# Performance work log

Hardware: AMD Instinct MI355X
Metric: run time of the kernel (lower is better)

## Reference

```python
import jax, jax.numpy as jnp
import numpy as np

D_MODEL = 512
N_HEAD = 8


def setup_inputs() -> dict:
    key = jax.random.key(0)
    ks = jax.random.split(key, 9)
    s = 1.0 / np.sqrt(D_MODEL)
    inp = {
        "x": jax.random.normal(ks[0], (2, 4096, D_MODEL), dtype=jnp.float32),
        "wq": jax.random.uniform(ks[1], (D_MODEL, D_MODEL), jnp.float32, -s, s),
        "bq": jax.random.uniform(ks[2], (D_MODEL,), jnp.float32, -s, s),
        "wk": jax.random.uniform(ks[3], (D_MODEL, D_MODEL), jnp.float32, -s, s),
        "bk": jax.random.uniform(ks[4], (D_MODEL,), jnp.float32, -s, s),
        "wv": jax.random.uniform(ks[5], (D_MODEL, D_MODEL), jnp.float32, -s, s),
        "bv": jax.random.uniform(ks[6], (D_MODEL,), jnp.float32, -s, s),
        "wo": jax.random.uniform(ks[7], (D_MODEL, D_MODEL), jnp.float32, -s, s),
        "bo": jax.random.uniform(ks[8], (D_MODEL,), jnp.float32, -s, s),
    }
    return inp


def reference(x, wq, bq, wk, bk, wv, bv, wo, bo):
    B, S, D = x.shape
    H = N_HEAD
    Dh = D // H

    def split_heads(t):  # [B,S,D] -> [B,H,S,Dh]
        return t.reshape(B, S, H, Dh).transpose(0, 2, 1, 3)

    q = split_heads(x @ wq.T + bq)
    k = split_heads(x @ wk.T + bk)
    v = split_heads(x @ wv.T + bv)

    # explicit (unfused) attention, matching the torch module
    score = jnp.einsum("bhsd,bhtd->bhst", q, k) / jnp.sqrt(jnp.float32(Dh))
    attn = jax.nn.softmax(score, axis=-1)
    out = jnp.einsum("bhst,bhtd->bhsd", attn, v)  # [B,H,S,Dh]

    out = out.transpose(0, 2, 1, 3).reshape(B, S, D)
    return out @ wo.T + bo
```

## Files before the change

### kernel.cpp

```cpp
#include <hip/hip_runtime.h>
#include <math.h>

#define S_LEN 4096
#define DMODEL 512
#define NHEAD 8
#define E_ELEMS ((size_t)8192 * 512)
#define QSCALE 0.18033688f

typedef __attribute__((ext_vector_type(8))) short bf16x8;
typedef __attribute__((ext_vector_type(4))) float f32x4;
typedef __attribute__((ext_vector_type(16))) float f32x16;
typedef unsigned short u16;
typedef unsigned int u32;

__device__ __forceinline__ u16 f2bf(float f) {
    u32 u = __float_as_uint(f);
    u += 0x7FFFu + ((u >> 16) & 1u);
    return (u16)(u >> 16);
}
__device__ __forceinline__ float bf2f(u16 h) {
    return __uint_as_float((u32)h << 16);
}

#define MFMA16(a, b, c) __builtin_amdgcn_mfma_f32_16x16x32_bf16((a), (b), (c), 0, 0, 0)
#define MFMA32(a, b, c) __builtin_amdgcn_mfma_f32_32x32x16_bf16((a), (b), (c), 0, 0, 0)

__global__ __launch_bounds__(256) void cvt_x(const float* __restrict__ in,
                                             u16* __restrict__ out, int n4) {
    const int i = blockIdx.x * 256 + threadIdx.x;
    if (i >= n4) return;
    const float4 v = ((const float4*)in)[i];
    uint2 hp;
    hp.x = (u32)f2bf(v.x) | ((u32)f2bf(v.y) << 16);
    hp.y = (u32)f2bf(v.z) | ((u32)f2bf(v.w) << 16);
    ((uint2*)out)[i] = hp;
}

__global__ __launch_bounds__(256) void cvt_w(
    const float* __restrict__ wq, const float* __restrict__ wk,
    const float* __restrict__ wv, const float* __restrict__ wo,
    u16* __restrict__ oq, u16* __restrict__ ok,
    u16* __restrict__ ov, u16* __restrict__ oo) {
    const int i = blockIdx.x * 256 + threadIdx.x;
    {
        const float4 v = ((const float4*)wq)[i];
        uint2 hp;
        hp.x = (u32)f2bf(v.x * QSCALE) | ((u32)f2bf(v.y * QSCALE) << 16);
        hp.y = (u32)f2bf(v.z * QSCALE) | ((u32)f2bf(v.w * QSCALE) << 16);
        ((uint2*)oq)[i] = hp;
    }
    {
        const float4 v = ((const float4*)wk)[i];
        uint2 hp;
        hp.x = (u32)f2bf(v.x) | ((u32)f2bf(v.y) << 16);
        hp.y = (u32)f2bf(v.z) | ((u32)f2bf(v.w) << 16);
        ((uint2*)ok)[i] = hp;
    }
    {
        const float4 v = ((const float4*)wv)[i];
        uint2 hp;
        hp.x = (u32)f2bf(v.x) | ((u32)f2bf(v.y) << 16);
        hp.y = (u32)f2bf(v.z) | ((u32)f2bf(v.w) << 16);
        ((uint2*)ov)[i] = hp;
    }
    {
        const float4 v = ((const float4*)wo)[i];
        uint2 hp;
        hp.x = (u32)f2bf(v.x) | ((u32)f2bf(v.y) << 16);
        hp.y = (u32)f2bf(v.z) | ((u32)f2bf(v.w) << 16);
        ((uint2*)oo)[i] = hp;
    }
}

template<int MODE>
__global__ __launch_bounds__(256) void proj2_kernel(
    const u16* __restrict__ Abf,
    const u16* __restrict__ W0, const float* __restrict__ Bi0,
    const u16* __restrict__ W1, const float* __restrict__ Bi1,
    u16* __restrict__ Qo, u16* __restrict__ Ko, float* __restrict__ Out)
{
    __shared__ __align__(16) u16 sm[16384];
    u16* As = sm;
    u16* Bs = sm + 8192;

    const int tid = threadIdx.x;
    const int w = tid >> 6, l = tid & 63, g = (l >> 4), c = l & 15;
    const int wr = w >> 1, wc = w & 1;
    const int bm = blockIdx.x * 128;
    const int n0 = blockIdx.y * 128;
    const int z = (MODE == 0) ? blockIdx.z : 0;
    const u16* W   = z ? W1 : W0;
    const float* Bi = z ? Bi1 : Bi0;
    const float bsc = (MODE == 0 && z == 0) ? QSCALE : 1.0f;

    const int sr = l >> 3;
    const int slot = l & 7;

    f32x4 acc[4][4];
    #pragma unroll
    for (int i = 0; i < 4; ++i)
        #pragma unroll
        for (int j = 0; j < 4; ++j) acc[i][j] = (f32x4){0.f, 0.f, 0.f, 0.f};

    #pragma unroll 1
    for (int kt = 0; kt < 8; ++kt) {
        const int k0 = kt * 64;
        __syncthreads();
        #pragma unroll
        for (int i = 0; i < 4; ++i) {
            const int row = i * 32 + w * 8 + sr;
            const int scol = (slot ^ (row & 7)) * 8;
            __builtin_amdgcn_global_load_lds(
                Abf + (size_t)(bm + row) * DMODEL + k0 + scol,
                As + (i * 32 + w * 8) * 64, 16, 0, 0);
            __builtin_amdgcn_global_load_lds(
                W + (size_t)(n0 + row) * DMODEL + k0 + scol,
                Bs + (i * 32 + w * 8) * 64, 16, 0, 0);
        }
        __syncthreads();

        #pragma unroll
        for (int kc = 0; kc < 2; ++kc) {
            bf16x8 a[4], b[4];
            #pragma unroll
            for (int mf = 0; mf < 4; ++mf) {
                const int ra = wr * 64 + mf * 16 + c;
                a[mf] = *(const bf16x8*)(As + ra * 64 + (((kc * 4 + g) ^ (ra & 7)) * 8));
            }
            #pragma unroll
            for (int nf = 0; nf < 4; ++nf) {
                const int rb = wc * 64 + nf * 16 + c;
                b[nf] = *(const bf16x8*)(Bs + rb * 64 + (((kc * 4 + g) ^ (rb & 7)) * 8));
            }
            #pragma unroll
            for (int mf = 0; mf < 4; ++mf)
                #pragma unroll
                for (int nf = 0; nf < 4; ++nf)
                    acc[mf][nf] = MFMA16(a[mf], b[nf], acc[mf][nf]);
        }
    }

    #pragma unroll
    for (int mf = 0; mf < 4; ++mf)
        #pragma unroll
        for (int nf = 0; nf < 4; ++nf) {
            const int n = n0 + wc * 64 + nf * 16 + c;
            const float bias = Bi[n] * bsc;
            #pragma unroll
            for (int r = 0; r < 4; ++r) {
                const int m = bm + wr * 64 + mf * 16 + 4 * g + r;
                const float v = acc[mf][nf][r] + bias;
                if (MODE == 1) {
                    Out[(size_t)m * DMODEL + n] = v;
                } else {
                    const int b = m >> 12, s = m & (S_LEN - 1);
                    const int hh = n >> 6, dd = n & 63;
                    const size_t o = ((size_t)((b * NHEAD + hh) * S_LEN + s)) * 64 + dd;
                    if (z == 0) Qo[o] = f2bf(v);
                    else        Ko[o] = f2bf(v);
                }
            }
        }
}

__global__ __launch_bounds__(256) void proj_v_kernel(
    const u16* __restrict__ Abf, const u16* __restrict__ Wv,
    const float* __restrict__ Bv, u16* __restrict__ Vt)
{
    __shared__ __align__(16) u16 sm[18432];
    u16* Ah = sm;
    u16* Bh = sm + 9216;

    const int tid = threadIdx.x;
    const int w = tid >> 6, lane = tid & 63, g = lane >> 4, c = lane & 15;
    const int bm = blockIdx.x * 128;
    const int n0 = blockIdx.y * 64;

    f32x4 acc[2][4];
    #pragma unroll
    for (int a = 0; a < 2; ++a)
        #pragma unroll
        for (int b = 0; b < 4; ++b) acc[a][b] = (f32x4){0.f, 0.f, 0.f, 0.f};

    #pragma unroll 1
    for (int kt = 0; kt < 8; ++kt) {
        const int k0 = kt * 64;
        __syncthreads();
        #pragma unroll
        for (int i = 0; i < 4; ++i) {
            const int slot = i * 256 + tid;
            const int r = slot >> 3, c8 = slot & 7;
            *(uint4*)(Ah + r * 72 + c8 * 8) =
                *(const uint4*)(Abf + (size_t)(bm + r) * DMODEL + k0 + c8 * 8);
        }
        #pragma unroll
        for (int i = 0; i < 2; ++i) {
            const int slot = i * 256 + tid;
            const int r = slot >> 3, c8 = slot & 7;
            *(uint4*)(Bh + r * 72 + c8 * 8) =
                *(const uint4*)(Wv + (size_t)(n0 + r) * DMODEL + k0 + c8 * 8);
        }
        __syncthreads();

        #pragma unroll
        for (int kc = 0; kc < 2; ++kc) {
            bf16x8 a[2], b[4];
            #pragma unroll
            for (int mf = 0; mf < 2; ++mf)
                a[mf] = *(const bf16x8*)(Ah + (w * 32 + mf * 16 + c) * 72 + kc * 32 + g * 8);
            #pragma unroll
            for (int nf = 0; nf < 4; ++nf)
                b[nf] = *(const bf16x8*)(Bh + (nf * 16 + c) * 72 + kc * 32 + g * 8);
            #pragma unroll
            for (int mf = 0; mf < 2; ++mf)
                #pragma unroll
                for (int nf = 0; nf < 4; ++nf)
                    acc[mf][nf] = MFMA16(a[mf], b[nf], acc[mf][nf]);
        }
    }

    __syncthreads();
    float* scr = (float*)sm;
    #pragma unroll
    for (int mf = 0; mf < 2; ++mf)
        #pragma unroll
        for (int nf = 0; nf < 4; ++nf) {
            const float bias = Bv[n0 + nf * 16 + c];
            #pragma unroll
            for (int r = 0; r < 4; ++r)
                scr[(w * 32 + mf * 16 + 4 * g + r) * 72 + nf * 16 + c] =
                    acc[mf][nf][r] + bias;
        }
    __syncthreads();
    const int d = tid & 63, sb = tid >> 6;
    const int b = bm >> 12, h = n0 >> 6;
    const size_t obase =
        ((size_t)((b * NHEAD + h) * 64 + d)) * S_LEN + (bm & (S_LEN - 1)) + sb * 32;
    u16 th[32];
    #pragma unroll
    for (int j = 0; j < 32; ++j)
        th[j] = f2bf(scr[(sb * 32 + j) * 72 + d]);
    #pragma unroll
    for (int q = 0; q < 4; ++q)
        *(uint4*)(Vt + obase + q * 8) = *(const uint4*)&th[q * 8];
}

__global__ __launch_bounds__(256, 2) void attn_kernel(
    const u16* __restrict__ Qb, const u16* __restrict__ Kb,
    const u16* __restrict__ Vt, u16* __restrict__ OpB, float* __restrict__ Lp)
{
    __shared__ __align__(16) u16 sm[16384];

    const int tid = threadIdx.x;
    const int w = tid >> 6, l = tid & 63;
    const int r0 = l & 31, hi = l >> 5;

    const int f = blockIdx.x;
    const int wg = (f & 7) * 128 + (f >> 3);
    const int bh = wg >> 6, kvq = (wg >> 4) & 3, qb = wg & 15;
    const int b = bh >> 3, h = bh & 7;

    const size_t hoff = (size_t)bh * S_LEN * 64;
    const int qw = qb * 256 + w * 64;
    const int kv0 = kvq * 1024;

    bf16x8 qf[2][4];
    #pragma unroll
    for (int qfi = 0; qfi < 2; ++qfi)
        #pragma unroll
        for (int kc = 0; kc < 4; ++kc)
            qf[qfi][kc] = *(const bf16x8*)(Qb + hoff +
                (size_t)(qw + qfi * 32 + r0) * 64 + kc * 16 + hi * 8);

    const int rbase = r0 * 64;
    int soff[4];
    #pragma unroll
    for (int j = 0; j < 4; ++j) soff[j] = ((2 * j + hi) ^ (r0 & 7)) * 8;

    const int srow0 = w * 16 + (l >> 3);
    const int slot  = l & 7;
    const int srow1 = srow0 + 8;
    const u16* srcK0 = Kb + hoff + (size_t)(kv0 + srow0) * 64 + ((slot ^ (srow0 & 7)) * 8);
    const u16* srcK1 = Kb + hoff + (size_t)(kv0 + srow1) * 64 + ((slot ^ (srow1 & 7)) * 8);
    const u16* srcV0 = Vt + ((size_t)bh * 64 + srow0) * S_LEN + kv0 + ((slot ^ (srow0 & 7)) * 8);
    const u16* srcV1 = Vt + ((size_t)bh * 64 + srow1) * S_LEN + kv0 + ((slot ^ (srow1 & 7)) * 8);

#define STAGE(bufb, t) do {                                                        \
        u16* kb_ = sm + (bufb) * 8192 + w * 1024;                                  \
        u16* vb_ = kb_ + 4096;                                                     \
        __builtin_amdgcn_global_load_lds(srcK0 + (size_t)(t) * 4096, kb_,       16, 0, 0); \
        __builtin_amdgcn_global_load_lds(srcK1 + (size_t)(t) * 4096, kb_ + 512, 16, 0, 0); \
        __builtin_amdgcn_global_load_lds(srcV0 + (size_t)(t) * 64,   vb_,       16, 0, 0); \
        __builtin_amdgcn_global_load_lds(srcV1 + (size_t)(t) * 64,   vb_ + 512, 16, 0, 0); \
    } while (0)

#define ZERO16 {0.f,0.f,0.f,0.f,0.f,0.f,0.f,0.f,0.f,0.f,0.f,0.f,0.f,0.f,0.f,0.f}
    f32x16 o00 = ZERO16, o01 = ZERO16, o10 = ZERO16, o11 = ZERO16;
    f32x16 laccA = ZERO16, laccB = ZERO16;

    STAGE(0, 0);
    __syncthreads();
    int buf = 0;

    #pragma unroll 1
    for (int t = 0; t < 16; ++t) {
        if (t + 1 < 16) STAGE(buf ^ 1, t + 1);

        const u16* Kb_s = sm + buf * 8192;
        const u16* Vb_s = Kb_s + 4096;

        bf16x8 pa0[4], pa1[4];
        #pragma unroll
        for (int kvf = 0; kvf < 2; ++kvf) {
            f32x16 sA = ZERO16, sB = ZERO16;
            __builtin_amdgcn_s_setprio(1);
            #pragma unroll
            for (int kc = 0; kc < 4; ++kc) {
                const bf16x8 k = *(const bf16x8*)(Kb_s + kvf * 2048 + rbase + soff[kc]);
                sA = MFMA32(k, qf[0][kc], sA);
                sB = MFMA32(k, qf[1][kc], sB);
            }
            __builtin_amdgcn_s_setprio(0);
            #pragma unroll
            for (int r = 0; r < 16; ++r) {
                sA[r] = __builtin_amdgcn_exp2f(sA[r]);
                sB[r] = __builtin_amdgcn_exp2f(sB[r]);
            }
            laccA += sA;
            laccB += sB;
            #pragma unroll
            for (int hf = 0; hf < 2; ++hf) {
                const int rb = hf * 8;
                u32 x0, y0, x1, y1;
                asm("v_cvt_pk_bf16_f32 %0, %1, %2" : "=v"(x0) : "v"(sA[rb+0]), "v"(sA[rb+1]));
                asm("v_cvt_pk_bf16_f32 %0, %1, %2" : "=v"(y0) : "v"(sA[rb+4]), "v"(sA[rb+5]));
                asm("v_cvt_pk_bf16_f32 %0, %1, %2" : "=v"(x1) : "v"(sA[rb+2]), "v"(sA[rb+3]));
                asm("v_cvt_pk_bf16_f32 %0, %1, %2" : "=v"(y1) : "v"(sA[rb+6]), "v"(sA[rb+7]));
                asm volatile("v_permlane32_swap_b32 %0, %1" : "+v"(x0), "+v"(y0));
                asm volatile("v_permlane32_swap_b32 %0, %1" : "+v"(x1), "+v"(y1));
                union { u32 u[4]; bf16x8 v; } PA;
                PA.u[0] = x0; PA.u[1] = x1; PA.u[2] = y0; PA.u[3] = y1;
                pa0[kvf * 2 + hf] = PA.v;
                asm("v_cvt_pk_bf16_f32 %0, %1, %2" : "=v"(x0) : "v"(sB[rb+0]), "v"(sB[rb+1]));
                asm("v_cvt_pk_bf16_f32 %0, %1, %2" : "=v"(y0) : "v"(sB[rb+4]), "v"(sB[rb+5]));
                asm("v_cvt_pk_bf16_f32 %0, %1, %2" : "=v"(x1) : "v"(sB[rb+2]), "v"(sB[rb+3]));
                asm("v_cvt_pk_bf16_f32 %0, %1, %2" : "=v"(y1) : "v"(sB[rb+6]), "v"(sB[rb+7]));
                asm volatile("v_permlane32_swap_b32 %0, %1" : "+v"(x0), "+v"(y0));
                asm volatile("v_permlane32_swap_b32 %0, %1" : "+v"(x1), "+v"(y1));
                union { u32 u[4]; bf16x8 v; } PB;
                PB.u[0] = x0; PB.u[1] = x1; PB.u[2] = y0; PB.u[3] = y1;
                pa1[kvf * 2 + hf] = PB.v;
            }
        }

        __builtin_amdgcn_s_setprio(1);
        #pragma unroll
        for (int kvc = 0; kvc < 4; ++kvc) {
            const bf16x8 v0 = *(const bf16x8*)(Vb_s + rbase + soff[kvc]);
            const bf16x8 v1 = *(const bf16x8*)(Vb_s + 2048 + rbase + soff[kvc]);
            o00 = MFMA32(pa0[kvc], v0, o00);
            o01 = MFMA32(pa0[kvc], v1, o01);
            o10 = MFMA32(pa1[kvc], v0, o10);
            o11 = MFMA32(pa1[kvc], v1, o11);
        }
        __builtin_amdgcn_s_setprio(0);

        __syncthreads();
        buf ^= 1;
    }
#undef STAGE

    float l0 = 0.f, l1 = 0.f;
    #pragma unroll
    for (int r = 0; r < 16; ++r) { l0 += laccA[r]; l1 += laccB[r]; }
    l0 += __shfl_xor(l0, 32);
    l1 += __shfl_xor(l1, 32);
    if (hi == 0) {
        Lp[((size_t)kvq * 16 + bh) * S_LEN + qw + r0]      = l0;
        Lp[((size_t)kvq * 16 + bh) * S_LEN + qw + 32 + r0] = l1;
    }

    u16* Ob = OpB + (size_t)kvq * E_ELEMS + (size_t)b * S_LEN * DMODEL;
    #pragma unroll
    for (int qfi = 0; qfi < 2; ++qfi)
        #pragma unroll
        for (int df = 0; df < 2; ++df) {
            #pragma unroll
            for (int r = 0; r < 16; ++r) {
                const float ov = qfi ? (df ? o11[r] : o10[r]) : (df ? o01[r] : o00[r]);
                const int q = qfi * 32 + (r & 3) + 8 * (r >> 2) + 4 * hi;
                Ob[(size_t)(qw + q) * DMODEL + h * 64 + df * 32 + r0] = f2bf(ov);
            }
        }
}

__global__ __launch_bounds__(256) void combine_kernel(
    const u16* __restrict__ Op, const float* __restrict__ Lp,
    u16* __restrict__ A)
{
    const int i = blockIdx.x * 256 + threadIdx.x;
    const int m = i >> 6;
    const int col = (i & 63) * 8;
    const int b = m >> 12, s = m & (S_LEN - 1), h = col >> 6;
    const int bh = b * 8 + h;

    float lt = 0.f;
    #pragma unroll
    for (int kq = 0; kq < 4; ++kq)
        lt += Lp[((size_t)kq * 16 + bh) * S_LEN + s];
    const float inv = 1.0f / lt;

    float acc[8] = {};
    #pragma unroll
    for (int kq = 0; kq < 4; ++kq) {
        const uint4 v = *(const uint4*)(Op + (size_t)kq * E_ELEMS + (size_t)m * DMODEL + col);
        const u16* p = (const u16*)&v;
        #pragma unroll
        for (int j = 0; j < 8; ++j) acc[j] += bf2f(p[j]);
    }
    u16 r[8];
    #pragma unroll
    for (int j = 0; j < 8; ++j) r[j] = f2bf(acc[j] * inv);
    *(uint4*)(A + (size_t)m * DMODEL + col) = *(const uint4*)r;
}

extern "C" void kernel_launch(void* const* d_in, const int* in_sizes, int n_in,
                              void* d_out, int out_size, void* d_ws, size_t ws_size,
                              hipStream_t stream)
{
    const float* x  = (const float*)d_in[0];
    const float* wq = (const float*)d_in[1];
    const float* bq = (const float*)d_in[2];
    const float* wk = (const float*)d_in[3];
    const float* bk = (const float*)d_in[4];
    const float* wv = (const float*)d_in[5];
    const float* bv = (const float*)d_in[6];
    const float* wo = (const float*)d_in[7];
    const float* bo = (const float*)d_in[8];

    u16* ws = (u16*)d_ws;
    const size_t E = E_ELEMS;
    u16* xbf  = ws;
    u16* Qbf  = ws + E;
    u16* Kbf  = ws + 2 * E;
    u16* Vtbf = ws + 3 * E;
    u16* wqbf = ws + 4 * E;
    u16* wkbf = wqbf + DMODEL * DMODEL;
    u16* wvbf = wkbf + DMODEL * DMODEL;
    u16* wobf = wvbf + DMODEL * DMODEL;
    u16* OpB  = wobf + DMODEL * DMODEL;
    float* Lp = (float*)(OpB + 4 * E);

    cvt_x<<<dim3(4096), 256, 0, stream>>>(x, xbf, (int)(E / 4));
    cvt_w<<<dim3(256), 256, 0, stream>>>(wq, wk, wv, wo, wqbf, wkbf, wvbf, wobf);

    proj2_kernel<0><<<dim3(64, 4, 2), 256, 0, stream>>>(
        xbf, wqbf, bq, wkbf, bk, Qbf, Kbf, nullptr);

    proj_v_kernel<<<dim3(64, 8), 256, 0, stream>>>(xbf, wvbf, bv, Vtbf);

    attn_kernel<<<dim3(1024), 256, 0, stream>>>(Qbf, Kbf, Vtbf, OpB, Lp);

    combine_kernel<<<dim3(2048), 256, 0, stream>>>(OpB, Lp, xbf);

    proj2_kernel<1><<<dim3(64, 4), 256, 0, stream>>>(
        xbf, wobf, bo, nullptr, nullptr, nullptr, nullptr, (float*)d_out);
}
```

Baseline: 139.4 us.

## Merge conversion kernels, fold V projection into QK GEMM, interleave PV MFMAs

```diff
diff --git a/kernel.cpp b/kernel.cpp
--- a/kernel.cpp
+++ b/kernel.cpp
@@ -25,50 +25,51 @@
 #define MFMA16(a, b, c) __builtin_amdgcn_mfma_f32_16x16x32_bf16((a), (b), (c), 0, 0, 0)
 #define MFMA32(a, b, c) __builtin_amdgcn_mfma_f32_32x32x16_bf16((a), (b), (c), 0, 0, 0)
 
-__global__ __launch_bounds__(256) void cvt_x(const float* __restrict__ in,
-                                             u16* __restrict__ out, int n4) {
-    const int i = blockIdx.x * 256 + threadIdx.x;
-    if (i >= n4) return;
-    const float4 v = ((const float4*)in)[i];
-    uint2 hp;
-    hp.x = (u32)f2bf(v.x) | ((u32)f2bf(v.y) << 16);
-    hp.y = (u32)f2bf(v.z) | ((u32)f2bf(v.w) << 16);
-    ((uint2*)out)[i] = hp;
-}
-
-__global__ __launch_bounds__(256) void cvt_w(
+__global__ __launch_bounds__(256) void cvt_all(
+    const float* __restrict__ x,
     const float* __restrict__ wq, const float* __restrict__ wk,
     const float* __restrict__ wv, const float* __restrict__ wo,
-    u16* __restrict__ oq, u16* __restrict__ ok,
-    u16* __restrict__ ov, u16* __restrict__ oo) {
-    const int i = blockIdx.x * 256 + threadIdx.x;
-    {
-        const float4 v = ((const float4*)wq)[i];
-        uint2 hp;
-        hp.x = (u32)f2bf(v.x * QSCALE) | ((u32)f2bf(v.y * QSCALE) << 16);
-        hp.y = (u32)f2bf(v.z * QSCALE) | ((u32)f2bf(v.w * QSCALE) << 16);
-        ((uint2*)oq)[i] = hp;
-    }
-    {
-        const float4 v = ((const float4*)wk)[i];
+    u16* __restrict__ xbf, u16* __restrict__ oq, u16* __restrict__ ok,
+    u16* __restrict__ ov, u16* __restrict__ oo)
+{
+    const int bid = blockIdx.x;
+    if (bid < 4096) {
+        const int i = bid * 256 + threadIdx.x;
+        const float4 v = ((const float4*)x)[i];
         uint2 hp;
         hp.x = (u32)f2bf(v.x) | ((u32)f2bf(v.y) << 16);
         hp.y = (u32)f2bf(v.z) | ((u32)f2bf(v.w) << 16);
-        ((uint2*)ok)[i] = hp;
-    }
-    {
-        const float4 v = ((const float4*)wv)[i];
-        uint2 hp;
-        hp.x = (u32)f2bf(v.x) | ((u32)f2bf(v.y) << 16);
-        hp.y = (u32)f2bf(v.z) | ((u32)f2bf(v.w) << 16);
-        ((uint2*)ov)[i] = hp;
-    }
-    {
-        const float4 v = ((const float4*)wo)[i];
-        uint2 hp;
-        hp.x = (u32)f2bf(v.x) | ((u32)f2bf(v.y) << 16);
-        hp.y = (u32)f2bf(v.z) | ((u32)f2bf(v.w) << 16);
-        ((uint2*)oo)[i] = hp;
+        ((uint2*)xbf)[i] = hp;
+    } else {
+        const int i = (bid - 4096) * 256 + threadIdx.x;
+        {
+            const float4 v = ((const float4*)wq)[i];
+            uint2 hp;
+            hp.x = (u32)f2bf(v.x * QSCALE) | ((u32)f2bf(v.y * QSCALE) << 16);
+            hp.y = (u32)f2bf(v.z * QSCALE) | ((u32)f2bf(v.w * QSCALE) << 16);
+            ((uint2*)oq)[i] = hp;
+        }
+        {
+            const float4 v = ((const float4*)wk)[i];
+            uint2 hp;
+            hp.x = (u32)f2bf(v.x) | ((u32)f2bf(v.y) << 16);
+            hp.y = (u32)f2bf(v.z) | ((u32)f2bf(v.w) << 16);
+            ((uint2*)ok)[i] = hp;
+        }
+        {
+            const float4 v = ((const float4*)wv)[i];
+            uint2 hp;
+            hp.x = (u32)f2bf(v.x) | ((u32)f2bf(v.y) << 16);
+            hp.y = (u32)f2bf(v.z) | ((u32)f2bf(v.w) << 16);
+            ((uint2*)ov)[i] = hp;
+        }
+        {
+            const float4 v = ((const float4*)wo)[i];
+            uint2 hp;
+            hp.x = (u32)f2bf(v.x) | ((u32)f2bf(v.y) << 16);
+            hp.y = (u32)f2bf(v.z) | ((u32)f2bf(v.w) << 16);
+            ((uint2*)oo)[i] = hp;
+        }
     }
 }
 
@@ -77,9 +78,11 @@
     const u16* __restrict__ Abf,
     const u16* __restrict__ W0, const float* __restrict__ Bi0,
     const u16* __restrict__ W1, const float* __restrict__ Bi1,
-    u16* __restrict__ Qo, u16* __restrict__ Ko, float* __restrict__ Out)
+    const u16* __restrict__ W2, const float* __restrict__ Bi2,
+    u16* __restrict__ Qo, u16* __restrict__ Ko, u16* __restrict__ Vt,
+    float* __restrict__ Out)
 {
-    __shared__ __align__(16) u16 sm[16384];
+    __shared__ __align__(16) u16 sm[18432];
     u16* As = sm;
     u16* Bs = sm + 8192;
 
@@ -89,8 +92,8 @@
     const int bm = blockIdx.x * 128;
     const int n0 = blockIdx.y * 128;
     const int z = (MODE == 0) ? blockIdx.z : 0;
-    const u16* W   = z ? W1 : W0;
-    const float* Bi = z ? Bi1 : Bi0;
+    const u16* W   = (z == 0) ? W0 : (z == 1) ? W1 : W2;
+    const float* Bi = (z == 0) ? Bi0 : (z == 1) ? Bi1 : Bi2;
     const float bsc = (MODE == 0 && z == 0) ? QSCALE : 1.0f;
 
     const int sr = l >> 3;
@@ -138,6 +141,41 @@
                 for (int nf = 0; nf < 4; ++nf)
                     acc[mf][nf] = MFMA16(a[mf], b[nf], acc[mf][nf]);
         }
+    }
+
+    if (MODE == 0 && z == 2) {
+        __syncthreads();
+        float* scr = (float*)sm;
+        const int d = tid & 63, sb = tid >> 6;
+        const int b = bm >> 12;
+        #pragma unroll
+        for (int pass = 0; pass < 2; ++pass) {
+            if (wc == pass) {
+                #pragma unroll
+                for (int mf = 0; mf < 4; ++mf)
+                    #pragma unroll
+                    for (int nf = 0; nf < 4; ++nf) {
+                        const float bias = Bi[n0 + pass * 64 + nf * 16 + c];
+                        #pragma unroll
+                        for (int r = 0; r < 4; ++r)
+                            scr[(wr * 64 + mf * 16 + 4 * g + r) * 72 + nf * 16 + c] =
+                                acc[mf][nf][r] + bias;
+                    }
+            }
+            __syncthreads();
+            const int hh = (n0 >> 6) + pass;
+            const size_t obase =
+                ((size_t)((b * NHEAD + hh) * 64 + d)) * S_LEN + (bm & (S_LEN - 1)) + sb * 32;
+            u16 th[32];
+            #pragma unroll
+            for (int j = 0; j < 32; ++j)
+                th[j] = f2bf(scr[(sb * 32 + j) * 72 + d]);
+            #pragma unroll
+            for (int q4 = 0; q4 < 4; ++q4)
+                *(uint4*)(Vt + obase + q4 * 8) = *(const uint4*)&th[q4 * 8];
+            __syncthreads();
+        }
+        return;
     }
 
     #pragma unroll
@@ -163,88 +201,6 @@
         }
 }
 
-__global__ __launch_bounds__(256) void proj_v_kernel(
-    const u16* __restrict__ Abf, const u16* __restrict__ Wv,
-    const float* __restrict__ Bv, u16* __restrict__ Vt)
-{
-    __shared__ __align__(16) u16 sm[18432];
-    u16* Ah = sm;
-    u16* Bh = sm + 9216;
-
-    const int tid = threadIdx.x;
-    const int w = tid >> 6, lane = tid & 63, g = lane >> 4, c = lane & 15;
-    const int bm = blockIdx.x * 128;
-    const int n0 = blockIdx.y * 64;
-
-    f32x4 acc[2][4];
-    #pragma unroll
-    for (int a = 0; a < 2; ++a)
-        #pragma unroll
-        for (int b = 0; b < 4; ++b) acc[a][b] = (f32x4){0.f, 0.f, 0.f, 0.f};
-
-    #pragma unroll 1
-    for (int kt = 0; kt < 8; ++kt) {
-        const int k0 = kt * 64;
-        __syncthreads();
-        #pragma unroll
-        for (int i = 0; i < 4; ++i) {
-            const int slot = i * 256 + tid;
-            const int r = slot >> 3, c8 = slot & 7;
-            *(uint4*)(Ah + r * 72 + c8 * 8) =
-                *(const uint4*)(Abf + (size_t)(bm + r) * DMODEL + k0 + c8 * 8);
-        }
-        #pragma unroll
-        for (int i = 0; i < 2; ++i) {
-            const int slot = i * 256 + tid;
-            const int r = slot >> 3, c8 = slot & 7;
-            *(uint4*)(Bh + r * 72 + c8 * 8) =
-                *(const uint4*)(Wv + (size_t)(n0 + r) * DMODEL + k0 + c8 * 8);
-        }
-        __syncthreads();
-
-        #pragma unroll
-        for (int kc = 0; kc < 2; ++kc) {
-            bf16x8 a[2], b[4];
-            #pragma unroll
-            for (int mf = 0; mf < 2; ++mf)
-                a[mf] = *(const bf16x8*)(Ah + (w * 32 + mf * 16 + c) * 72 + kc * 32 + g * 8);
-            #pragma unroll
-            for (int nf = 0; nf < 4; ++nf)
-                b[nf] = *(const bf16x8*)(Bh + (nf * 16 + c) * 72 + kc * 32 + g * 8);
-            #pragma unroll
-            for (int mf = 0; mf < 2; ++mf)
-                #pragma unroll
-                for (int nf = 0; nf < 4; ++nf)
-                    acc[mf][nf] = MFMA16(a[mf], b[nf], acc[mf][nf]);
-        }
-    }
-
-    __syncthreads();
-    float* scr = (float*)sm;
-    #pragma unroll
-    for (int mf = 0; mf < 2; ++mf)
-        #pragma unroll
-        for (int nf = 0; nf < 4; ++nf) {
-            const float bias = Bv[n0 + nf * 16 + c];
-            #pragma unroll
-            for (int r = 0; r < 4; ++r)
-                scr[(w * 32 + mf * 16 + 4 * g + r) * 72 + nf * 16 + c] =
-                    acc[mf][nf][r] + bias;
-        }
-    __syncthreads();
-    const int d = tid & 63, sb = tid >> 6;
-    const int b = bm >> 12, h = n0 >> 6;
-    const size_t obase =
-        ((size_t)((b * NHEAD + h) * 64 + d)) * S_LEN + (bm & (S_LEN - 1)) + sb * 32;
-    u16 th[32];
-    #pragma unroll
-    for (int j = 0; j < 32; ++j)
-        th[j] = f2bf(scr[(sb * 32 + j) * 72 + d]);
-    #pragma unroll
-    for (int q = 0; q < 4; ++q)
-        *(uint4*)(Vt + obase + q * 8) = *(const uint4*)&th[q * 8];
-}
-
 __global__ __launch_bounds__(256, 2) void attn_kernel(
     const u16* __restrict__ Qb, const u16* __restrict__ Kb,
     const u16* __restrict__ Vt, u16* __restrict__ OpB, float* __restrict__ Lp)
@@ -296,7 +252,7 @@
 
 #define ZERO16 {0.f,0.f,0.f,0.f,0.f,0.f,0.f,0.f,0.f,0.f,0.f,0.f,0.f,0.f,0.f,0.f}
     f32x16 o00 = ZERO16, o01 = ZERO16, o10 = ZERO16, o11 = ZERO16;
-    f32x16 laccA = ZERO16, laccB = ZERO16;
+    float lA = 0.f, lB = 0.f;
 
     STAGE(0, 0);
     __syncthreads();
@@ -309,7 +265,6 @@
         const u16* Kb_s = sm + buf * 8192;
         const u16* Vb_s = Kb_s + 4096;
 
-        bf16x8 pa0[4], pa1[4];
         #pragma unroll
         for (int kvf = 0; kvf < 2; ++kvf) {
             f32x16 sA = ZERO16, sB = ZERO16;
@@ -321,16 +276,19 @@
                 sB = MFMA32(k, qf[1][kc], sB);
             }
             __builtin_amdgcn_s_setprio(0);
+
             #pragma unroll
             for (int r = 0; r < 16; ++r) {
                 sA[r] = __builtin_amdgcn_exp2f(sA[r]);
                 sB[r] = __builtin_amdgcn_exp2f(sB[r]);
             }
-            laccA += sA;
-            laccB += sB;
+            #pragma unroll
+            for (int r = 0; r < 16; ++r) { lA += sA[r]; lB += sB[r]; }
+
             #pragma unroll
             for (int hf = 0; hf < 2; ++hf) {
                 const int rb = hf * 8;
+                const int idx = kvf * 2 + hf;
                 u32 x0, y0, x1, y1;
                 asm("v_cvt_pk_bf16_f32 %0, %1, %2" : "=v"(x0) : "v"(sA[rb+0]), "v"(sA[rb+1]));
                 asm("v_cvt_pk_bf16_f32 %0, %1, %2" : "=v"(y0) : "v"(sA[rb+4]), "v"(sA[rb+5]));
@@ -340,7 +298,6 @@
                 asm volatile("v_permlane32_swap_b32 %0, %1" : "+v"(x1), "+v"(y1));
                 union { u32 u[4]; bf16x8 v; } PA;
                 PA.u[0] = x0; PA.u[1] = x1; PA.u[2] = y0; PA.u[3] = y1;
-                pa0[kvf * 2 + hf] = PA.v;
                 asm("v_cvt_pk_bf16_f32 %0, %1, %2" : "=v"(x0) : "v"(sB[rb+0]), "v"(sB[rb+1]));
                 asm("v_cvt_pk_bf16_f32 %0, %1, %2" : "=v"(y0) : "v"(sB[rb+4]), "v"(sB[rb+5]));
                 asm("v_cvt_pk_bf16_f32 %0, %1, %2" : "=v"(x1) : "v"(sB[rb+2]), "v"(sB[rb+3]));
@@ -349,35 +306,28 @@
                 asm volatile("v_permlane32_swap_b32 %0, %1" : "+v"(x1), "+v"(y1));
                 union { u32 u[4]; bf16x8 v; } PB;
                 PB.u[0] = x0; PB.u[1] = x1; PB.u[2] = y0; PB.u[3] = y1;
-                pa1[kvf * 2 + hf] = PB.v;
-            }
-        }
-
-        __builtin_amdgcn_s_setprio(1);
-        #pragma unroll
-        for (int kvc = 0; kvc < 4; ++kvc) {
-            const bf16x8 v0 = *(const bf16x8*)(Vb_s + rbase + soff[kvc]);
-            const bf16x8 v1 = *(const bf16x8*)(Vb_s + 2048 + rbase + soff[kvc]);
-            o00 = MFMA32(pa0[kvc], v0, o00);
-            o01 = MFMA32(pa0[kvc], v1, o01);
-            o10 = MFMA32(pa1[kvc], v0, o10);
-            o11 = MFMA32(pa1[kvc], v1, o11);
-        }
-        __builtin_amdgcn_s_setprio(0);
+
+                const bf16x8 v0 = *(const bf16x8*)(Vb_s + rbase + soff[idx]);
+                const bf16x8 v1 = *(const bf16x8*)(Vb_s + 2048 + rbase + soff[idx]);
+                __builtin_amdgcn_s_setprio(1);
+                o00 = MFMA32(PA.v, v0, o00);
+                o01 = MFMA32(PA.v, v1, o01);
+                o10 = MFMA32(PB.v, v0, o10);
+                o11 = MFMA32(PB.v, v1, o11);
+                __builtin_amdgcn_s_setprio(0);
+            }
+        }
 
         __syncthreads();
         buf ^= 1;
     }
 #undef STAGE
 
-    float l0 = 0.f, l1 = 0.f;
-    #pragma unroll
-    for (int r = 0; r < 16; ++r) { l0 += laccA[r]; l1 += laccB[r]; }
-    l0 += __shfl_xor(l0, 32);
-    l1 += __shfl_xor(l1, 32);
+    lA += __shfl_xor(lA, 32);
+    lB += __shfl_xor(lB, 32);
     if (hi == 0) {
-        Lp[((size_t)kvq * 16 + bh) * S_LEN + qw + r0]      = l0;
-        Lp[((size_t)kvq * 16 + bh) * S_LEN + qw + 32 + r0] = l1;
+        Lp[((size_t)kvq * 16 + bh) * S_LEN + qw + r0]      = lA;
+        Lp[((size_t)kvq * 16 + bh) * S_LEN + qw + 32 + r0] = lB;
     }
 
     u16* Ob = OpB + (size_t)kvq * E_ELEMS + (size_t)b * S_LEN * DMODEL;
@@ -451,18 +401,17 @@
     u16* OpB  = wobf + DMODEL * DMODEL;
     float* Lp = (float*)(OpB + 4 * E);
 
-    cvt_x<<<dim3(4096), 256, 0, stream>>>(x, xbf, (int)(E / 4));
-    cvt_w<<<dim3(256), 256, 0, stream>>>(wq, wk, wv, wo, wqbf, wkbf, wvbf, wobf);
-
-    proj2_kernel<0><<<dim3(64, 4, 2), 256, 0, stream>>>(
-        xbf, wqbf, bq, wkbf, bk, Qbf, Kbf, nullptr);
-
-    proj_v_kernel<<<dim3(64, 8), 256, 0, stream>>>(xbf, wvbf, bv, Vtbf);
+    cvt_all<<<dim3(4352), 256, 0, stream>>>(
+        x, wq, wk, wv, wo, xbf, wqbf, wkbf, wvbf, wobf);
+
+    proj2_kernel<0><<<dim3(64, 4, 3), 256, 0, stream>>>(
+        xbf, wqbf, bq, wkbf, bk, wvbf, bv, Qbf, Kbf, Vtbf, nullptr);
 
     attn_kernel<<<dim3(1024), 256, 0, stream>>>(Qbf, Kbf, Vtbf, OpB, Lp);
 
     combine_kernel<<<dim3(2048), 256, 0, stream>>>(OpB, Lp, xbf);
 
-    proj2_kernel<1><<<dim3(64, 4), 256, 0, stream>>>(
-        xbf, wobf, bo, nullptr, nullptr, nullptr, nullptr, (float*)d_out);
-}
+    proj2_kernel<1><<<dim3(64, 4, 1), 256, 0, stream>>>(
+        xbf, wobf, bo, nullptr, nullptr, nullptr, nullptr,
+        nullptr, nullptr, nullptr, (float*)d_out);
+}
```

Measured after the change: 130.5 us. 6.4% less time.
